# Performance work log

Measured on AMD Instinct MI355X. Metric: run time of the kernel, lower is better.

## Reference

```python
import jax, jax.numpy as jnp
import numpy as np

IN_FEATURES = 1024
OUT_FEATURES = 1024
GRID_SIZE = 5
SPLINE_ORDER = 3
GRID_RANGE = (-1.0, 1.0)
BATCH = 8192


def setup_inputs() -> dict:
    key = jax.random.key(0)
    k1, k2, k3, k4 = jax.random.split(key, 4)
    x = jax.random.uniform(k1, (BATCH, IN_FEATURES), dtype=jnp.float32)  # in [0,1) c grid_range
    base_weight = jax.random.normal(k2, (OUT_FEATURES, IN_FEATURES), dtype=jnp.float32) * 0.04
    spline_weight = jax.random.normal(k3, (OUT_FEATURES, IN_FEATURES, GRID_SIZE + SPLINE_ORDER), dtype=jnp.float32) * 0.05
    spline_scaler = jax.random.normal(k4, (OUT_FEATURES, IN_FEATURES), dtype=jnp.float32) * 0.04
    # non-trainable grid buffer, matches tf.range(-k, G+k+1)*h + lo tiled over in_features
    h = (GRID_RANGE[1] - GRID_RANGE[0]) / GRID_SIZE
    g = jnp.arange(-SPLINE_ORDER, GRID_SIZE + SPLINE_ORDER + 1, dtype=jnp.float32) * h + GRID_RANGE[0]
    grid = jnp.tile(g[None, :], (IN_FEATURES, 1))  # [in, G+2k+1]
    return {"x": x, "base_weight": base_weight, "spline_weight": spline_weight,
            "spline_scaler": spline_scaler, "grid": grid}


def b_splines(x, grid):
    # x: [B, in]; grid: [in, G+2k+1] -> bases: [B, in, G+k]
    xe = x[..., None]
    bases = jnp.logical_and(xe >= grid[:, :-1], xe < grid[:, 1:]).astype(x.dtype)
    for k in range(1, SPLINE_ORDER + 1):
        left = (xe - grid[:, :-(k + 1)]) / (grid[:, k:-1] - grid[:, :-(k + 1)])
        right = (grid[:, k + 1:] - xe) / (grid[:, k + 1:] - grid[:, 1:-k])
        bases = left * bases[..., :-1] + right * bases[..., 1:]
    return bases


def reference(x, base_weight, spline_weight, spline_scaler, grid):
    base_out = jnp.matmul(jax.nn.silu(x), base_weight.T)  # [B, out]
    ssw = spline_weight * spline_scaler[..., None]          # [out, in, G+k]
    bs = b_splines(x, grid).reshape(x.shape[0], -1)         # [B, in*(G+k)]
    spline_out = jnp.matmul(bs, ssw.reshape(OUT_FEATURES, -1).T)  # [B, out]
    return base_out + spline_out
```

## Files before the change

kernel.cpp:

```cpp
#include <hip/hip_runtime.h>
#include <hip/hip_bf16.h>
#include <math.h>

#define IN_F  1024
#define OUT_F 1024
#define BATCH 8192
#define KD2   7168
#define KHALF 3584
#define NKS   56
#define HTSH  8192
#define HT2   (2 * HTSH)
#define RPB   4

typedef short short8  __attribute__((ext_vector_type(8)));
typedef short short4v __attribute__((ext_vector_type(4)));
typedef float f32x4   __attribute__((ext_vector_type(4)));

__device__ __forceinline__ short f2bf(float f) {
    __hip_bfloat16 h = __float2bfloat16(f);
    return *reinterpret_cast<short*>(&h);
}

__device__ __forceinline__ float silu(float v) {
    return v / (1.0f + __expf(-v));
}

__device__ __forceinline__ size_t tile_off(int rowblk, int kh, int ks, int half) {
    return (((((size_t)rowblk * 2 + kh) * NKS + ks) * 2) + half) * (size_t)HTSH;
}

__device__ __forceinline__ void bases6(float xv, short* __restrict__ o) {
    const float s  = (xv + 2.2f) * 2.5f;
    const float cf = floorf(s);
    const int  off = (int)cf - 5;
    const float u  = s - cf, um = 1.0f - u;
    const float u2 = u * u, u3 = u2 * u, um3 = um * um * um;
    const float k6 = 0.16666667f;
    const float w0 = um3 * k6;
    const float w1 = (3.0f * u3 - 6.0f * u2 + 4.0f) * k6;
    const float w2 = (-3.0f * u3 + 3.0f * u2 + 3.0f * u + 1.0f) * k6;
    const float w3 = u3 * k6;
    o[0] = f2bf(off == 0 ? w0 : 0.0f);
    o[1] = f2bf(off == 0 ? w1 : (off == 1 ? w0 : 0.0f));
    o[2] = f2bf(off == 0 ? w2 : (off == 1 ? w1 : w0));
    o[3] = f2bf(off == 0 ? w3 : (off == 1 ? w2 : w1));
    o[4] = f2bf(off == 1 ? w3 : (off == 2 ? w2 : 0.0f));
    o[5] = f2bf(off == 2 ? w3 : 0.0f);
}

__device__ __forceinline__ void scatter4(const short (*buf)[KD2], short* mat,
                                         int r0, int q) {
    const int rowblk = r0 >> 8;
    const int half   = (r0 >> 7) & 1;
    const int rlb    = r0 & 127;
#pragma unroll
    for (int it = 0; it < 14; ++it) {
        const int g  = it * 256 + q;
        const int t  = g >> 5;
        const int rr = (g >> 3) & 3;
        const int c8 = g & 7;
        const int kh = t >= NKS;
        const int ks = t - kh * NKS;
        const int rl = rlb + rr;
        const int col = (c8 * 8) ^ ((rl & 7) << 3);
        *(short8*)&mat[tile_off(rowblk, kh, ks, half) + (size_t)rl * 64 + col] =
            *(const short8*)&buf[rr][t * 64 + c8 * 8];
    }
}

__global__ __launch_bounds__(256)
void pack_A(const float* __restrict__ x, short* __restrict__ A) {
    __shared__ short buf[RPB][KD2];
    const int r0 = blockIdx.x * RPB;
    const int q  = threadIdx.x;
#pragma unroll
    for (int rr = 0; rr < RPB; ++rr) {
        const float4 xv = *(const float4*)&x[(size_t)(r0 + rr) * IN_F + q * 4];
        short t[24];
        bases6(xv.x, t + 0);
        bases6(xv.y, t + 6);
        bases6(xv.z, t + 12);
        bases6(xv.w, t + 18);
        *(short8*)&buf[rr][q * 24 + 0]  = *(short8*)(t + 0);
        *(short8*)&buf[rr][q * 24 + 8]  = *(short8*)(t + 8);
        *(short8*)&buf[rr][q * 24 + 16] = *(short8*)(t + 16);
        short4v sl;
        sl[0] = f2bf(silu(xv.x)); sl[1] = f2bf(silu(xv.y));
        sl[2] = f2bf(silu(xv.z)); sl[3] = f2bf(silu(xv.w));
        *(short4v*)&buf[rr][6144 + q * 4] = sl;
    }
    __syncthreads();
    scatter4(buf, A, r0, q);
}

__global__ __launch_bounds__(256)
void pack_W(const float* __restrict__ base_w, const float* __restrict__ spline_w,
            const float* __restrict__ scaler, short* __restrict__ Wt) {
    __shared__ short buf[RPB][KD2];
    const int o0 = blockIdx.x * RPB;
    const int q  = threadIdx.x;
#pragma unroll
    for (int rr = 0; rr < RPB; ++rr) {
        const int row = o0 + rr;
        const int i0  = q * 4;
        short t[24];
#pragma unroll
        for (int f = 0; f < 4; ++f) {
            const size_t idx = (size_t)row * IN_F + i0 + f;
            const float sc = scaler[idx];
            const float4* sw4 = (const float4*)(spline_w + idx * 8);
            const float4 w0 = sw4[0], w1 = sw4[1];
            t[f * 6 + 0] = f2bf(w0.z * sc);
            t[f * 6 + 1] = f2bf(w0.w * sc);
            t[f * 6 + 2] = f2bf(w1.x * sc);
            t[f * 6 + 3] = f2bf(w1.y * sc);
            t[f * 6 + 4] = f2bf(w1.z * sc);
            t[f * 6 + 5] = f2bf(w1.w * sc);
        }
        *(short8*)&buf[rr][q * 24 + 0]  = *(short8*)(t + 0);
        *(short8*)&buf[rr][q * 24 + 8]  = *(short8*)(t + 8);
        *(short8*)&buf[rr][q * 24 + 16] = *(short8*)(t + 16);
        const float4 bw = *(const float4*)&base_w[(size_t)row * IN_F + i0];
        short4v bv;
        bv[0] = f2bf(bw.x); bv[1] = f2bf(bw.y);
        bv[2] = f2bf(bw.z); bv[3] = f2bf(bw.w);
        *(short4v*)&buf[rr][6144 + q * 4] = bv;
    }
    __syncthreads();
    scatter4(buf, Wt, o0, q);
}

#define GLD_LDS16(gp, lp)                                                     \
    __builtin_amdgcn_global_load_lds(                                         \
        (const __attribute__((address_space(1))) unsigned int*)(gp),          \
        (__attribute__((address_space(3))) unsigned int*)(lp), 16, 0, 0)

#define STG2(p_, db_, hf_, arr_)                                              \
    GLD_LDS16((p_) + (hf_) * HTSH,       &arr_[db_][hf_][wave * 1024]);       \
    GLD_LDS16((p_) + (hf_) * HTSH + 512, &arr_[db_][hf_][wave * 1024 + 512]);

#define STG4(p_, db_, arr_)                                                   \
    STG2(p_, db_, 0, arr_); STG2(p_, db_, 1, arr_);

#define LDA(db_, m_, kf_) (*(const short8*)&As[db_][wr]                       \
    [((m_) * 16 + lrow) * 64 + (((kf_) * 32 + quad * 8) ^ swz)])
#define LDB(db_, n_, kf_) (*(const short8*)&Bs[db_][bhalf]                    \
    [(bro + (n_) * 16 + lrow) * 64 + (((kf_) * 32 + quad * 8) ^ swz)])

#define RD_A(mh_, db_) {                                                      \
    _Pragma("unroll")                                                         \
    for (int m_ = 0; m_ < 4; ++m_) {                                          \
        af[m_][0] = LDA(db_, (mh_) * 4 + m_, 0);                              \
        af[m_][1] = LDA(db_, (mh_) * 4 + m_, 1);                              \
    } }
#define RD_B(db_) {                                                           \
    _Pragma("unroll")                                                         \
    for (int n_ = 0; n_ < 4; ++n_) {                                          \
        bf[n_][0] = LDB(db_, n_, 0);                                          \
        bf[n_][1] = LDB(db_, n_, 1);                                          \
    } }

#define MQ32(mo_)                                                             \
    _Pragma("unroll")                                                         \
    for (int m_ = 0; m_ < 4; ++m_)                                            \
    _Pragma("unroll")                                                         \
    for (int n_ = 0; n_ < 4; ++n_)                                            \
    _Pragma("unroll")                                                         \
    for (int kf_ = 0; kf_ < 2; ++kf_)                                         \
        acc[(mo_) + m_][n_] = __builtin_amdgcn_mfma_f32_16x16x32_bf16(        \
            af[m_][kf_], bf[n_][kf_], acc[(mo_) + m_][n_], 0, 0, 0);

#define CFENCE asm volatile("" ::: "memory")
#define BAR   do { CFENCE; __builtin_amdgcn_s_barrier(); CFENCE; } while (0)
#define PRIO1 __builtin_amdgcn_s_setprio(1)
#define PRIO0 __builtin_amdgcn_s_setprio(0)
#define VM4   asm volatile("s_waitcnt vmcnt(4)" ::: "memory")
#define VM8   asm volatile("s_waitcnt vmcnt(8)" ::: "memory")

__global__ __launch_bounds__(512, 2)
void kan_gemm8(const short* __restrict__ A, const short* __restrict__ Wt,
               float* __restrict__ out0, float* __restrict__ out1) {
    __shared__ short As[2][2][HTSH];
    __shared__ short Bs[2][2][HTSH];

    const int bid = blockIdx.x;
    const int xcd = bid & 7;
    const int j   = bid >> 3;
    const int kh  = xcd >> 2;
    const int cbp = (xcd >> 1) & 1;
    const int rbh = xcd & 1;
    const int rb  = rbh * 16 + (j >> 1);
    const int cb  = cbp * 2 + (j & 1);

    const int tid   = threadIdx.x;
    const int lane  = tid & 63;
    const int wave  = tid >> 6;
    const int wr    = wave & 1;
    const int wc    = wave >> 1;
    const int bhalf = wc >> 1;
    const int bro   = (wc & 1) * 64;
    const int lrow  = lane & 15;
    const int quad  = lane >> 4;
    const int swz   = (lrow & 7) << 3;

    float* __restrict__ outp = kh ? out1 : out0;

    f32x4 acc[8][4];
#pragma unroll
    for (int i = 0; i < 8; ++i)
#pragma unroll
        for (int n = 0; n < 4; ++n) acc[i][n] = (f32x4)0.0f;

    short8 af[4][2], bf[4][2];

    const short* pA = A  + tile_off(rb, kh, 0, 0) + wave * 1024 + lane * 8;
    const short* pB = Wt + tile_off(cb, kh, 0, 0) + wave * 1024 + lane * 8;

    STG4(pA, 0, As);
    STG4(pB, 0, Bs);
    STG4(pA + HT2, 1, As);
    STG4(pB + HT2, 1, Bs);
    VM8;
    BAR;
    RD_A(0, 0); RD_B(0);

    for (int it = 0; it < NKS / 2; ++it) {
        STG4(pB + 2 * HT2, 0, Bs);
        BAR; PRIO1; MQ32(0); RD_A(1, 0); PRIO0; BAR;
        VM4;
        STG4(pA + 2 * HT2, 0, As);
        BAR; PRIO1; MQ32(4); RD_A(0, 1); RD_B(1); PRIO0; BAR;
        STG4(pB + 3 * HT2, 1, Bs);
        BAR; PRIO1; MQ32(0); RD_A(1, 1); PRIO0; BAR;
        VM4;
        STG4(pA + 3 * HT2, 1, As);
        BAR; PRIO1; MQ32(4); RD_A(0, 0); RD_B(0); PRIO0; BAR;
        pA += 2 * HT2; pB += 2 * HT2;
    }

    const int row0 = rb * 256 + wr * 128;
    const int col0 = cb * 256 + wc * 64;
#pragma unroll
    for (int i = 0; i < 8; ++i)
#pragma unroll
        for (int n = 0; n < 4; ++n)
#pragma unroll
            for (int r = 0; r < 4; ++r)
                outp[(size_t)(row0 + i * 16 + quad * 4 + r) * OUT_F +
                     (col0 + n * 16 + lrow)] = acc[i][n][r];
}

__global__ __launch_bounds__(256)
void reduce_add(float* __restrict__ out, const float* __restrict__ part) {
    const size_t i = ((size_t)blockIdx.x * 256 + threadIdx.x) * 4;
    float4 a = *(float4*)&out[i];
    const float4 b = *(const float4*)&part[i];
    a.x += b.x; a.y += b.y; a.z += b.z; a.w += b.w;
    *(float4*)&out[i] = a;
}

#define BM 128
#define BN 128
#define STF 40

__device__ __forceinline__ short8 bases8(float xv) {
    const float s  = (xv + 2.2f) * 2.5f;
    const float cf = floorf(s);
    const int   ci = (int)cf;
    const float u  = s - cf, um = 1.0f - u;
    const float u2 = u * u, u3 = u2 * u, um3 = um * um * um;
    const float k6 = 0.16666667f;
    const float w0 = um3 * k6;
    const float w1 = (3.0f * u3 - 6.0f * u2 + 4.0f) * k6;
    const float w2 = (-3.0f * u3 + 3.0f * u2 + 3.0f * u + 1.0f) * k6;
    const float w3 = u3 * k6;
    short8 o;
#pragma unroll
    for (int j = 0; j < 8; ++j) {
        const float v5 = (j == 2) ? w0 : (j == 3) ? w1 : (j == 4) ? w2 : (j == 5) ? w3 : 0.0f;
        const float v6 = (j == 3) ? w0 : (j == 4) ? w1 : (j == 5) ? w2 : (j == 6) ? w3 : 0.0f;
        const float v7 = (j == 4) ? w0 : (j == 5) ? w1 : (j == 6) ? w2 : (j == 7) ? w3 : 0.0f;
        o[j] = f2bf((ci == 5) ? v5 : (ci == 6) ? v6 : v7);
    }
    return o;
}

__global__ __launch_bounds__(256)
void kan_mfma(const float* __restrict__ x,
              const float* __restrict__ base_w,
              const float* __restrict__ spline_w,
              const float* __restrict__ scaler,
              float* __restrict__ out) {
    __shared__ short As2[BM * STF];
    __shared__ short Bs2[BN * STF];

    const int tid  = threadIdx.x;
    const int lane = tid & 63;
    const int wave = tid >> 6;
    const int row0 = blockIdx.y * BM;
    const int col0 = blockIdx.x * BN;
    const int wm0  = (wave & 1) * 64;
    const int wn0  = (wave >> 1) * 64;
    const int lrow = lane & 15;
    const int quad = lane >> 4;

    f32x4 acc[4][4];
#pragma unroll
    for (int i = 0; i < 4; ++i)
#pragma unroll
        for (int j = 0; j < 4; ++j) acc[i][j] = (f32x4)0.0f;

    for (int kc = 0; kc < 256; ++kc) {
        const int fi0 = kc * 4;
#pragma unroll
        for (int it = 0; it < 2; ++it) {
            const int e = tid + it * 256;
            const int r = e >> 2, f = e & 3;
            const float xv = x[(size_t)(row0 + r) * IN_F + fi0 + f];
            *(short8*)&As2[r * STF + f * 8] = bases8(xv);
        }
#pragma unroll
        for (int it = 0; it < 4; ++it) {
            const int idx = tid + it * 256;
            const int c = idx >> 3, qq = idx & 7;
            const int f = qq >> 1;
            const size_t base = ((size_t)(col0 + c) * IN_F + fi0 + f) * 8 + (size_t)(qq & 1) * 4;
            const float4 w = *(const float4*)&spline_w[base];
            const float sc = scaler[(size_t)(col0 + c) * IN_F + fi0 + f];
            short4v o;
            o[0] = f2bf(w.x * sc); o[1] = f2bf(w.y * sc);
            o[2] = f2bf(w.z * sc); o[3] = f2bf(w.w * sc);
            *(short4v*)&Bs2[c * STF + qq * 4] = o;
        }
        __syncthreads();
        short8 a[4], b[4];
#pragma unroll
        for (int i = 0; i < 4; ++i)
            a[i] = *(const short8*)&As2[(wm0 + i * 16 + lrow) * STF + quad * 8];
#pragma unroll
        for (int i = 0; i < 4; ++i)
            b[i] = *(const short8*)&Bs2[(wn0 + i * 16 + lrow) * STF + quad * 8];
#pragma unroll
        for (int i = 0; i < 4; ++i)
#pragma unroll
            for (int j = 0; j < 4; ++j)
                acc[i][j] = __builtin_amdgcn_mfma_f32_16x16x32_bf16(a[i], b[j], acc[i][j], 0, 0, 0);
        __syncthreads();
    }

    for (int sc = 0; sc < 32; ++sc) {
        const int fi0 = sc * 32;
#pragma unroll
        for (int it = 0; it < 4; ++it) {
            const int idx = tid + it * 256;
            const int r = idx >> 3, qq = idx & 7;
            const float4 xv = *(const float4*)&x[(size_t)(row0 + r) * IN_F + fi0 + qq * 4];
            short4v o;
            o[0] = f2bf(silu(xv.x)); o[1] = f2bf(silu(xv.y));
            o[2] = f2bf(silu(xv.z)); o[3] = f2bf(silu(xv.w));
            *(short4v*)&As2[r * STF + qq * 4] = o;
        }
#pragma unroll
        for (int it = 0; it < 4; ++it) {
            const int idx = tid + it * 256;
            const int c = idx >> 3, qq = idx & 7;
            const float4 wv = *(const float4*)&base_w[(size_t)(col0 + c) * IN_F + fi0 + qq * 4];
            short4v o;
            o[0] = f2bf(wv.x); o[1] = f2bf(wv.y);
            o[2] = f2bf(wv.z); o[3] = f2bf(wv.w);
            *(short4v*)&Bs2[c * STF + qq * 4] = o;
        }
        __syncthreads();
        short8 a[4], b[4];
#pragma unroll
        for (int i = 0; i < 4; ++i)
            a[i] = *(const short8*)&As2[(wm0 + i * 16 + lrow) * STF + quad * 8];
#pragma unroll
        for (int i = 0; i < 4; ++i)
            b[i] = *(const short8*)&Bs2[(wn0 + i * 16 + lrow) * STF + quad * 8];
#pragma unroll
        for (int i = 0; i < 4; ++i)
#pragma unroll
            for (int j = 0; j < 4; ++j)
                acc[i][j] = __builtin_amdgcn_mfma_f32_16x16x32_bf16(a[i], b[j], acc[i][j], 0, 0, 0);
        __syncthreads();
    }

#pragma unroll
    for (int i = 0; i < 4; ++i)
#pragma unroll
        for (int j = 0; j < 4; ++j)
#pragma unroll
            for (int r = 0; r < 4; ++r)
                out[(size_t)(row0 + wm0 + i * 16 + quad * 4 + r) * OUT_F +
                    (col0 + wn0 + j * 16 + lrow)] = acc[i][j][r];
}

extern "C" void kernel_launch(void* const* d_in, const int* in_sizes, int n_in,
                              void* d_out, int out_size, void* d_ws, size_t ws_size,
                              hipStream_t stream) {
    const float* x        = (const float*)d_in[0];
    const float* base_w   = (const float*)d_in[1];
    const float* spline_w = (const float*)d_in[2];
    const float* scaler   = (const float*)d_in[3];
    float* out = (float*)d_out;

    const size_t need_A = (size_t)BATCH * KD2 * sizeof(short);
    const size_t need_W = (size_t)OUT_F * KD2 * sizeof(short);
    const size_t need_P = (size_t)BATCH * OUT_F * sizeof(float);

    if (ws_size >= need_A + need_W + need_P) {
        short* A  = (short*)d_ws;
        short* Wt = (short*)((char*)d_ws + need_A);
        float* P  = (float*)((char*)d_ws + need_A + need_W);
        pack_A<<<BATCH / RPB, 256, 0, stream>>>(x, A);
        pack_W<<<OUT_F / RPB, 256, 0, stream>>>(base_w, spline_w, scaler, Wt);
        kan_gemm8<<<256, 512, 0, stream>>>(A, Wt, out, P);
        reduce_add<<<BATCH * OUT_F / 1024, 256, 0, stream>>>(out, P);
    } else {
        dim3 grd(OUT_F / BN, BATCH / BM);
        kan_mfma<<<grd, 256, 0, stream>>>(x, base_w, spline_w, scaler, out);
    }
}
```

Baseline: 250.2 us.

## Merge pack kernels and shrink GEMM tiles to 128x128 with 1024 blocks

Fuses the A and W packing kernels into one launch that branches on block index. It also replaces the 256x256-tile, 512-thread split-K GEMM with a 128x128-tile, 256-thread kernel over 1024 blocks. The aim is to remove one launch and raise occupancy and CU coverage. The cost is lower data reuse per tile and more global traffic for A and B.

```diff
diff --git a/kernel.cpp b/kernel.cpp
--- a/kernel.cpp
+++ b/kernel.cpp
@@ -69,65 +69,64 @@
 }
 
 __global__ __launch_bounds__(256)
-void pack_A(const float* __restrict__ x, short* __restrict__ A) {
+void pack_all4(const float* __restrict__ x, const float* __restrict__ base_w,
+               const float* __restrict__ spline_w, const float* __restrict__ scaler,
+               short* __restrict__ A, short* __restrict__ Wt) {
     __shared__ short buf[RPB][KD2];
-    const int r0 = blockIdx.x * RPB;
-    const int q  = threadIdx.x;
-#pragma unroll
-    for (int rr = 0; rr < RPB; ++rr) {
-        const float4 xv = *(const float4*)&x[(size_t)(r0 + rr) * IN_F + q * 4];
-        short t[24];
-        bases6(xv.x, t + 0);
-        bases6(xv.y, t + 6);
-        bases6(xv.z, t + 12);
-        bases6(xv.w, t + 18);
-        *(short8*)&buf[rr][q * 24 + 0]  = *(short8*)(t + 0);
-        *(short8*)&buf[rr][q * 24 + 8]  = *(short8*)(t + 8);
-        *(short8*)&buf[rr][q * 24 + 16] = *(short8*)(t + 16);
-        short4v sl;
-        sl[0] = f2bf(silu(xv.x)); sl[1] = f2bf(silu(xv.y));
-        sl[2] = f2bf(silu(xv.z)); sl[3] = f2bf(silu(xv.w));
-        *(short4v*)&buf[rr][6144 + q * 4] = sl;
-    }
-    __syncthreads();
-    scatter4(buf, A, r0, q);
-}
-
-__global__ __launch_bounds__(256)
-void pack_W(const float* __restrict__ base_w, const float* __restrict__ spline_w,
-            const float* __restrict__ scaler, short* __restrict__ Wt) {
-    __shared__ short buf[RPB][KD2];
-    const int o0 = blockIdx.x * RPB;
-    const int q  = threadIdx.x;
-#pragma unroll
-    for (int rr = 0; rr < RPB; ++rr) {
-        const int row = o0 + rr;
-        const int i0  = q * 4;
-        short t[24];
-#pragma unroll
-        for (int f = 0; f < 4; ++f) {
-            const size_t idx = (size_t)row * IN_F + i0 + f;
-            const float sc = scaler[idx];
-            const float4* sw4 = (const float4*)(spline_w + idx * 8);
-            const float4 w0 = sw4[0], w1 = sw4[1];
-            t[f * 6 + 0] = f2bf(w0.z * sc);
-            t[f * 6 + 1] = f2bf(w0.w * sc);
-            t[f * 6 + 2] = f2bf(w1.x * sc);
-            t[f * 6 + 3] = f2bf(w1.y * sc);
-            t[f * 6 + 4] = f2bf(w1.z * sc);
-            t[f * 6 + 5] = f2bf(w1.w * sc);
-        }
-        *(short8*)&buf[rr][q * 24 + 0]  = *(short8*)(t + 0);
-        *(short8*)&buf[rr][q * 24 + 8]  = *(short8*)(t + 8);
-        *(short8*)&buf[rr][q * 24 + 16] = *(short8*)(t + 16);
-        const float4 bw = *(const float4*)&base_w[(size_t)row * IN_F + i0];
-        short4v bv;
-        bv[0] = f2bf(bw.x); bv[1] = f2bf(bw.y);
-        bv[2] = f2bf(bw.z); bv[3] = f2bf(bw.w);
-        *(short4v*)&buf[rr][6144 + q * 4] = bv;
-    }
-    __syncthreads();
-    scatter4(buf, Wt, o0, q);
+    const int b = blockIdx.x;
+    const int q = threadIdx.x;
+    if (b < BATCH / RPB) {
+        const int r0 = b * RPB;
+#pragma unroll
+        for (int rr = 0; rr < RPB; ++rr) {
+            const float4 xv = *(const float4*)&x[(size_t)(r0 + rr) * IN_F + q * 4];
+            short t[24];
+            bases6(xv.x, t + 0);
+            bases6(xv.y, t + 6);
+            bases6(xv.z, t + 12);
+            bases6(xv.w, t + 18);
+            *(short8*)&buf[rr][q * 24 + 0]  = *(short8*)(t + 0);
+            *(short8*)&buf[rr][q * 24 + 8]  = *(short8*)(t + 8);
+            *(short8*)&buf[rr][q * 24 + 16] = *(short8*)(t + 16);
+            short4v sl;
+            sl[0] = f2bf(silu(xv.x)); sl[1] = f2bf(silu(xv.y));
+            sl[2] = f2bf(silu(xv.z)); sl[3] = f2bf(silu(xv.w));
+            *(short4v*)&buf[rr][6144 + q * 4] = sl;
+        }
+        __syncthreads();
+        scatter4(buf, A, r0, q);
+    } else {
+        const int o0 = (b - BATCH / RPB) * RPB;
+#pragma unroll
+        for (int rr = 0; rr < RPB; ++rr) {
+            const int row = o0 + rr;
+            const int i0  = q * 4;
+            short t[24];
+#pragma unroll
+            for (int f = 0; f < 4; ++f) {
+                const size_t idx = (size_t)row * IN_F + i0 + f;
+                const float sc = scaler[idx];
+                const float4* sw4 = (const float4*)(spline_w + idx * 8);
+                const float4 w0 = sw4[0], w1 = sw4[1];
+                t[f * 6 + 0] = f2bf(w0.z * sc);
+                t[f * 6 + 1] = f2bf(w0.w * sc);
+                t[f * 6 + 2] = f2bf(w1.x * sc);
+                t[f * 6 + 3] = f2bf(w1.y * sc);
+                t[f * 6 + 4] = f2bf(w1.z * sc);
+                t[f * 6 + 5] = f2bf(w1.w * sc);
+            }
+            *(short8*)&buf[rr][q * 24 + 0]  = *(short8*)(t + 0);
+            *(short8*)&buf[rr][q * 24 + 8]  = *(short8*)(t + 8);
+            *(short8*)&buf[rr][q * 24 + 16] = *(short8*)(t + 16);
+            const float4 bw = *(const float4*)&base_w[(size_t)row * IN_F + i0];
+            short4v bv;
+            bv[0] = f2bf(bw.x); bv[1] = f2bf(bw.y);
+            bv[2] = f2bf(bw.z); bv[3] = f2bf(bw.w);
+            *(short4v*)&buf[rr][6144 + q * 4] = bv;
+        }
+        __syncthreads();
+        scatter4(buf, Wt, o0, q);
+    }
 }
 
 #define GLD_LDS16(gp, lp)                                                     \
@@ -135,23 +134,22 @@
         (const __attribute__((address_space(1))) unsigned int*)(gp),          \
         (__attribute__((address_space(3))) unsigned int*)(lp), 16, 0, 0)
 
-#define STG2(p_, db_, hf_, arr_)                                              \
-    GLD_LDS16((p_) + (hf_) * HTSH,       &arr_[db_][hf_][wave * 1024]);       \
-    GLD_LDS16((p_) + (hf_) * HTSH + 512, &arr_[db_][hf_][wave * 1024 + 512]);
-
 #define STG4(p_, db_, arr_)                                                   \
-    STG2(p_, db_, 0, arr_); STG2(p_, db_, 1, arr_);
-
-#define LDA(db_, m_, kf_) (*(const short8*)&As[db_][wr]                       \
-    [((m_) * 16 + lrow) * 64 + (((kf_) * 32 + quad * 8) ^ swz)])
-#define LDB(db_, n_, kf_) (*(const short8*)&Bs[db_][bhalf]                    \
-    [(bro + (n_) * 16 + lrow) * 64 + (((kf_) * 32 + quad * 8) ^ swz)])
-
-#define RD_A(mh_, db_) {                                                      \
+    GLD_LDS16((p_),        &arr_[db_][0 * 2048 + wave * 512]);                \
+    GLD_LDS16((p_) + 2048, &arr_[db_][1 * 2048 + wave * 512]);                \
+    GLD_LDS16((p_) + 4096, &arr_[db_][2 * 2048 + wave * 512]);                \
+    GLD_LDS16((p_) + 6144, &arr_[db_][3 * 2048 + wave * 512]);
+
+#define LDA(db_, m_, kf_) (*(const short8*)&As[db_]                           \
+    [(wm0 + (m_) * 16 + lrow) * 64 + (((kf_) * 32 + quad * 8) ^ swz)])
+#define LDB(db_, n_, kf_) (*(const short8*)&Bs[db_]                           \
+    [(wn0 + (n_) * 16 + lrow) * 64 + (((kf_) * 32 + quad * 8) ^ swz)])
+
+#define RD_A(db_) {                                                           \
     _Pragma("unroll")                                                         \
     for (int m_ = 0; m_ < 4; ++m_) {                                          \
-        af[m_][0] = LDA(db_, (mh_) * 4 + m_, 0);                              \
-        af[m_][1] = LDA(db_, (mh_) * 4 + m_, 1);                              \
+        af[m_][0] = LDA(db_, m_, 0);                                          \
+        af[m_][1] = LDA(db_, m_, 1);                                          \
     } }
 #define RD_B(db_) {                                                           \
     _Pragma("unroll")                                                         \
@@ -160,15 +158,16 @@
         bf[n_][1] = LDB(db_, n_, 1);                                          \
     } }
 
-#define MQ32(mo_)                                                             \
+#define MQ16(nh_)                                                             \
     _Pragma("unroll")                                                         \
     for (int m_ = 0; m_ < 4; ++m_)                                            \
     _Pragma("unroll")                                                         \
-    for (int n_ = 0; n_ < 4; ++n_)                                            \
+    for (int n_ = 0; n_ < 2; ++n_)                                            \
     _Pragma("unroll")                                                         \
     for (int kf_ = 0; kf_ < 2; ++kf_)                                         \
-        acc[(mo_) + m_][n_] = __builtin_amdgcn_mfma_f32_16x16x32_bf16(        \
-            af[m_][kf_], bf[n_][kf_], acc[(mo_) + m_][n_], 0, 0, 0);
+        acc[m_][(nh_) * 2 + n_] = __builtin_amdgcn_mfma_f32_16x16x32_bf16(    \
+            af[m_][kf_], bf[(nh_) * 2 + n_][kf_], acc[m_][(nh_) * 2 + n_],    \
+            0, 0, 0);
 
 #define CFENCE asm volatile("" ::: "memory")
 #define BAR   do { CFENCE; __builtin_amdgcn_s_barrier(); CFENCE; } while (0)
@@ -177,44 +176,41 @@
 #define VM4   asm volatile("s_waitcnt vmcnt(4)" ::: "memory")
 #define VM8   asm volatile("s_waitcnt vmcnt(8)" ::: "memory")
 
-__global__ __launch_bounds__(512, 2)
-void kan_gemm8(const short* __restrict__ A, const short* __restrict__ Wt,
+__global__ __launch_bounds__(256, 2)
+void kan_gemm2(const short* __restrict__ A, const short* __restrict__ Wt,
                float* __restrict__ out0, float* __restrict__ out1) {
-    __shared__ short As[2][2][HTSH];
-    __shared__ short Bs[2][2][HTSH];
+    __shared__ short As[2][HTSH];
+    __shared__ short Bs[2][HTSH];
 
     const int bid = blockIdx.x;
     const int xcd = bid & 7;
     const int j   = bid >> 3;
     const int kh  = xcd >> 2;
-    const int cbp = (xcd >> 1) & 1;
-    const int rbh = xcd & 1;
-    const int rb  = rbh * 16 + (j >> 1);
-    const int cb  = cbp * 2 + (j & 1);
-
-    const int tid   = threadIdx.x;
-    const int lane  = tid & 63;
-    const int wave  = tid >> 6;
-    const int wr    = wave & 1;
-    const int wc    = wave >> 1;
-    const int bhalf = wc >> 1;
-    const int bro   = (wc & 1) * 64;
-    const int lrow  = lane & 15;
-    const int quad  = lane >> 4;
-    const int swz   = (lrow & 7) << 3;
+    const int cbq = xcd & 3;
+    const int cb  = cbq * 2 + (j & 1);
+    const int rb  = j >> 1;
+
+    const int tid  = threadIdx.x;
+    const int lane = tid & 63;
+    const int wave = tid >> 6;
+    const int wm0  = (wave & 1) * 64;
+    const int wn0  = (wave >> 1) * 64;
+    const int lrow = lane & 15;
+    const int quad = lane >> 4;
+    const int swz  = (lrow & 7) << 3;
 
     float* __restrict__ outp = kh ? out1 : out0;
 
-    f32x4 acc[8][4];
-#pragma unroll
-    for (int i = 0; i < 8; ++i)
+    f32x4 acc[4][4];
+#pragma unroll
+    for (int i = 0; i < 4; ++i)
 #pragma unroll
         for (int n = 0; n < 4; ++n) acc[i][n] = (f32x4)0.0f;
 
     short8 af[4][2], bf[4][2];
 
-    const short* pA = A  + tile_off(rb, kh, 0, 0) + wave * 1024 + lane * 8;
-    const short* pB = Wt + tile_off(cb, kh, 0, 0) + wave * 1024 + lane * 8;
+    const short* pA = A  + tile_off(rb >> 1, kh, 0, rb & 1) + tid * 8;
+    const short* pB = Wt + tile_off(cb >> 1, kh, 0, cb & 1) + tid * 8;
 
     STG4(pA, 0, As);
     STG4(pB, 0, Bs);
@@ -222,32 +218,32 @@
     STG4(pB + HT2, 1, Bs);
     VM8;
     BAR;
-    RD_A(0, 0); RD_B(0);
+    RD_A(0); RD_B(0);
 
     for (int it = 0; it < NKS / 2; ++it) {
         STG4(pB + 2 * HT2, 0, Bs);
-        BAR; PRIO1; MQ32(0); RD_A(1, 0); PRIO0; BAR;
+        BAR; PRIO1; MQ16(0); PRIO0; BAR;
         VM4;
         STG4(pA + 2 * HT2, 0, As);
-        BAR; PRIO1; MQ32(4); RD_A(0, 1); RD_B(1); PRIO0; BAR;
+        BAR; PRIO1; MQ16(1); RD_A(1); RD_B(1); PRIO0; BAR;
         STG4(pB + 3 * HT2, 1, Bs);
-        BAR; PRIO1; MQ32(0); RD_A(1, 1); PRIO0; BAR;
+        BAR; PRIO1; MQ16(0); PRIO0; BAR;
         VM4;
         STG4(pA + 3 * HT2, 1, As);
-        BAR; PRIO1; MQ32(4); RD_A(0, 0); RD_B(0); PRIO0; BAR;
+        BAR; PRIO1; MQ16(1); RD_A(0); RD_B(0); PRIO0; BAR;
         pA += 2 * HT2; pB += 2 * HT2;
     }
 
-    const int row0 = rb * 256 + wr * 128;
-    const int col0 = cb * 256 + wc * 64;
-#pragma unroll
-    for (int i = 0; i < 8; ++i)
+    const int row0 = rb * 128 + wm0;
+    const int col0 = cb * 128 + wn0;
+#pragma unroll
+    for (int m = 0; m < 4; ++m)
 #pragma unroll
         for (int n = 0; n < 4; ++n)
 #pragma unroll
             for (int r = 0; r < 4; ++r)
-                outp[(size_t)(row0 + i * 16 + quad * 4 + r) * OUT_F +
-                     (col0 + n * 16 + lrow)] = acc[i][n][r];
+                outp[(size_t)(row0 + m * 16 + quad * 4 + r) * OUT_F +
+                     (col0 + n * 16 + lrow)] = acc[m][n][r];
 }
 
 __global__ __launch_bounds__(256)
@@ -413,9 +409,9 @@
         short* A  = (short*)d_ws;
         short* Wt = (short*)((char*)d_ws + need_A);
         float* P  = (float*)((char*)d_ws + need_A + need_W);
-        pack_A<<<BATCH / RPB, 256, 0, stream>>>(x, A);
-        pack_W<<<OUT_F / RPB, 256, 0, stream>>>(base_w, spline_w, scaler, Wt);
-        kan_gemm8<<<256, 512, 0, stream>>>(A, Wt, out, P);
+        pack_all4<<<BATCH / RPB + OUT_F / RPB, 256, 0, stream>>>(
+            x, base_w, spline_w, scaler, A, Wt);
+        kan_gemm2<<<1024, 256, 0, stream>>>(A, Wt, out, P);
         reduce_add<<<BATCH * OUT_F / 1024, 256, 0, stream>>>(out, P);
     } else {
         dim3 grd(OUT_F / BN, BATCH / BM);
```

Measured after the change: 265.6 us. +6.2%, slower.
